# Optimization experiments

Measured on AMD Instinct MI355X. Metric: run time of the kernel, lower is better.

The kernel has to match this reference:

```python
import jax, jax.numpy as jnp
import numpy as np

NL, NH, H, FF, V, P = 12, 12, 768, 3072, 30522, 512
B, L, S = 4, 512, 8
DH = H // NH


def _layer_norm(x, g, b, eps=1e-12):
    m = x.mean(-1, keepdims=True)
    v = jnp.mean((x - m) ** 2, axis=-1, keepdims=True)
    return (x - m) * jax.lax.rsqrt(v + eps) * g + b


def setup_inputs() -> dict:
    key = jax.random.key(0)
    ks = iter(jax.random.split(key, 40))
    pm = lambda shape: jax.random.normal(next(ks), shape, jnp.float32) * 0.02
    inp = {
        'word_emb': pm((V, H)), 'pos_emb': pm((P, H)), 'type_emb': pm((2, H)),
        'emb_ln_g': jnp.ones((H,), jnp.float32), 'emb_ln_b': jnp.zeros((H,), jnp.float32),
        'Wq': pm((NL, H, H)), 'bq': jnp.zeros((NL, H), jnp.float32),
        'Wk': pm((NL, H, H)), 'bk': jnp.zeros((NL, H), jnp.float32),
        'Wv': pm((NL, H, H)), 'bv': jnp.zeros((NL, H), jnp.float32),
        'Wo': pm((NL, H, H)), 'bo': jnp.zeros((NL, H), jnp.float32),
        'attn_ln_g': jnp.ones((NL, H), jnp.float32), 'attn_ln_b': jnp.zeros((NL, H), jnp.float32),
        'W1': pm((NL, H, FF)), 'b1': jnp.zeros((NL, FF), jnp.float32),
        'W2': pm((NL, FF, H)), 'b2': jnp.zeros((NL, H), jnp.float32),
        'ffn_ln_g': jnp.ones((NL, H), jnp.float32), 'ffn_ln_b': jnp.zeros((NL, H), jnp.float32),
        'fc_w': pm((H,)), 'fc_b': jnp.zeros((), jnp.float32),
    }
    inp['input_ids'] = jax.random.randint(next(ks), (B, L), 0, V)
    inp['token_type_ids'] = jnp.zeros((B, L), jnp.int32)
    # valid-length prefix attention_mask and sorted bos_locations (history = 64)
    vl = np.array([384 + 16 * (i % 8) for i in range(B)])
    hist = 64
    am = (np.arange(L)[None, :] < vl[:, None]).astype(np.int32)
    bos = np.stack([hist + (np.arange(S) * (v - hist)) // S for v in vl]).astype(np.int64)
    inp['attention_mask'] = jnp.asarray(am)
    inp['bos_locations'] = jnp.asarray(bos)
    return inp


def _forward(word_emb, pos_emb, type_emb, emb_ln_g, emb_ln_b,
             Wq, bq, Wk, bk, Wv, bv, Wo, bo, attn_ln_g, attn_ln_b,
             W1, b1, W2, b2, ffn_ln_g, ffn_ln_b, fc_w, fc_b,
             input_ids, token_type_ids, attention_mask, bos_locations):
    Bs, Ls = input_ids.shape
    t = jnp.arange(Ls)
    valid_len = attention_mask.sum(-1)                       # [B]
    hist = bos_locations[:, 0]                               # [B] history length
    # segment id per token: number of bos positions <= t, minus 1 (-1 in history)
    seg = (bos_locations[:, :, None] <= t[None, None, :]).sum(1) - 1   # [B,L]
    valid = t[None, :] < valid_len[:, None]                  # [B,L]
    # block-diagonal candidate attention mask (history rows/cols fully visible)
    p = t[None, :, None]
    q = t[None, None, :]
    hist_pq = (p < hist[:, None, None]) | (q < hist[:, None, None])
    same_seg = seg[:, :, None] == seg[:, None, :]
    mask = valid[:, :, None] & valid[:, None, :] & (hist_pq | same_seg)  # [B,L,L]
    bias = jnp.where(mask, 0.0, -10000.0).astype(jnp.float32)[:, None, :, :]  # [B,1,L,L]

    # BERT embeddings
    x = word_emb[input_ids] + pos_emb[t][None] + type_emb[token_type_ids]
    x = _layer_norm(x, emb_ln_g, emb_ln_b)
    scale = 1.0 / jnp.sqrt(jnp.asarray(DH, x.dtype))

    for l in range(NL):
        qh = (x @ Wq[l] + bq[l]).reshape(Bs, Ls, NH, DH)
        kh = (x @ Wk[l] + bk[l]).reshape(Bs, Ls, NH, DH)
        vh = (x @ Wv[l] + bv[l]).reshape(Bs, Ls, NH, DH)
        scores = jnp.einsum('bqhd,bkhd->bhqk', qh, kh) * scale + bias
        probs = jax.nn.softmax(scores, axis=-1)
        ctx = jnp.einsum('bhqk,bkhd->bqhd', probs, vh).reshape(Bs, Ls, H)
        x = _layer_norm(x + ctx @ Wo[l] + bo[l], attn_ln_g[l], attn_ln_b[l])
        h = jax.nn.gelu(x @ W1[l] + b1[l], approximate=False)
        x = _layer_norm(x + h @ W2[l] + b2[l], ffn_ln_g[l], ffn_ln_b[l])

    # variable-length segment mean pooling via membership matmul
    starts = bos_locations                                   # [B,S]
    ends = jnp.concatenate([bos_locations[:, 1:], valid_len[:, None]], axis=1)
    memb = ((t[None, None, :] >= starts[:, :, None]) &
            (t[None, None, :] < ends[:, :, None])).astype(x.dtype)        # [B,S,L]
    pooled = jnp.einsum('bsl,bld->bsd', memb, x) / memb.sum(-1, keepdims=True)
    logits = pooled @ fc_w + fc_b                            # [B,S]
    return jnp.squeeze(logits)


def reference(word_emb, pos_emb, type_emb, emb_ln_g, emb_ln_b,
              Wq, bq, Wk, bk, Wv, bv, Wo, bo, attn_ln_g, attn_ln_b,
              W1, b1, W2, b2, ffn_ln_g, ffn_ln_b, fc_w, fc_b,
              input_ids, token_type_ids, attention_mask, bos_locations):
    return _forward(word_emb, pos_emb, type_emb, emb_ln_g, emb_ln_b,
                    Wq, bq, Wk, bk, Wv, bv, Wo, bo, attn_ln_g, attn_ln_b,
                    W1, b1, W2, b2, ffn_ln_g, ffn_ln_b, fc_w, fc_b,
                    input_ids, token_type_ids, attention_mask, bos_locations)
```

## Files before the change

### kernel.cpp

```cpp
#include <hip/hip_runtime.h>
#include <math.h>

#define HH 768
#define FF 3072
#define NL 12
#define NH 12
#define DH 64
#define BB 4
#define LL 512
#define SS 8
#define MM (BB*LL)
#define WQSZ (HH*HH)
#define W1SZ (HH*FF)
#define LWB 7077888
#define OFF_WO 1769472
#define OFF_W1 2359296
#define OFF_W2 4718592

typedef short bf16x8 __attribute__((ext_vector_type(8)));
typedef float f32x4 __attribute__((ext_vector_type(4)));

__device__ inline ushort f2b(float f) {
  unsigned u = __float_as_uint(f);
  unsigned r = (u + 0x7FFFu + ((u >> 16) & 1u)) >> 16;
  return (ushort)r;
}

__device__ inline void swz_xy(int& x, int& y) {
  int gx = gridDim.x, gy = gridDim.y;
  int flat = blockIdx.x + blockIdx.y * gx;
  int nwg = gx * gy;
  int q = nwg >> 3, r = nwg & 7;
  int xcd = flat & 7, off = flat >> 3;
  int wgid = (xcd < r ? xcd * (q + 1) : r * (q + 1) + (xcd - r) * q) + off;
  x = wgid / gy; y = wgid - x * gy;
}

__global__ void prep_kernel(const int* __restrict__ am, const int* __restrict__ bos,
                            int* __restrict__ seg, int* __restrict__ vl) {
  int b = blockIdx.x;
  int t = threadIdx.x;
  __shared__ int red[512];
  red[t] = am[b*LL + t];
  __syncthreads();
  for (int off = 256; off > 0; off >>= 1) {
    if (t < off) red[t] += red[t+off];
    __syncthreads();
  }
  if (t == 0) vl[b] = red[0];
  int cnt = 0;
  #pragma unroll
  for (int s = 0; s < SS; s++) cnt += (bos[b*SS + s] <= t) ? 1 : 0;
  seg[b*LL + t] = cnt - 1;
}

__global__ __launch_bounds__(256) void embed_ln_kernel(
    const float* __restrict__ word_emb, const float* __restrict__ pos_emb,
    const float* __restrict__ type_emb, const float* __restrict__ g,
    const float* __restrict__ bta, const int* __restrict__ ids,
    const int* __restrict__ tts, float* __restrict__ x, ushort* __restrict__ xb)
{
  int row = blockIdx.x;
  int l = row & (LL-1);
  int t = threadIdx.x;
  int id = ids[row];
  int ty = tts[row];
  float4 v = {0.f,0.f,0.f,0.f};
  float s = 0.f, sq = 0.f;
  int c = t << 2;
  if (t < 192) {
    float4 a = *(const float4*)&word_emb[(size_t)id*HH + c];
    float4 p = *(const float4*)&pos_emb[l*HH + c];
    float4 ttv = *(const float4*)&type_emb[ty*HH + c];
    v.x = a.x+p.x+ttv.x; v.y = a.y+p.y+ttv.y; v.z = a.z+p.z+ttv.z; v.w = a.w+p.w+ttv.w;
    s = v.x+v.y+v.z+v.w;
    sq = v.x*v.x+v.y*v.y+v.z*v.z+v.w*v.w;
  }
  __shared__ float rs[256], rq[256];
  rs[t] = s; rq[t] = sq;
  __syncthreads();
  for (int off = 128; off > 0; off >>= 1) {
    if (t < off) { rs[t] += rs[t+off]; rq[t] += rq[t+off]; }
    __syncthreads();
  }
  float mean = rs[0] / HH;
  float var  = rq[0] / HH - mean*mean;
  float inv  = rsqrtf(var + 1e-12f);
  if (t < 192) {
    float4 gv = *(const float4*)&g[c];
    float4 bv = *(const float4*)&bta[c];
    float4 o;
    o.x = (v.x-mean)*inv*gv.x + bv.x;
    o.y = (v.y-mean)*inv*gv.y + bv.y;
    o.z = (v.z-mean)*inv*gv.z + bv.z;
    o.w = (v.w-mean)*inv*gv.w + bv.w;
    *(float4*)&x[(size_t)row*HH + c] = o;
    ushort4 ob = { f2b(o.x), f2b(o.y), f2b(o.z), f2b(o.w) };
    *(ushort4*)&xb[(size_t)row*HH + c] = ob;
  }
}

template<int NP>
__global__ __launch_bounds__(256) void add_ln_kernel(
    const float* __restrict__ xin, const float* __restrict__ y,
    const float* __restrict__ g, const float* __restrict__ bta,
    float* __restrict__ xout, ushort* __restrict__ xb)
{
  int row = blockIdx.x;
  int t = threadIdx.x;
  float4 v = {0.f,0.f,0.f,0.f};
  float s = 0.f, sq = 0.f;
  int c = t << 2;
  size_t ix = (size_t)row*HH + c;
  if (t < 192) {
    v = *(const float4*)&xin[ix];
    #pragma unroll
    for (int p = 0; p < NP; p++) {
      float4 yv = *(const float4*)&y[(size_t)p*MM*HH + ix];
      v.x += yv.x; v.y += yv.y; v.z += yv.z; v.w += yv.w;
    }
    s = v.x+v.y+v.z+v.w;
    sq = v.x*v.x+v.y*v.y+v.z*v.z+v.w*v.w;
  }
  __shared__ float rs[256], rq[256];
  rs[t] = s; rq[t] = sq;
  __syncthreads();
  for (int off = 128; off > 0; off >>= 1) {
    if (t < off) { rs[t] += rs[t+off]; rq[t] += rq[t+off]; }
    __syncthreads();
  }
  float mean = rs[0] / HH;
  float var  = rq[0] / HH - mean*mean;
  float inv  = rsqrtf(var + 1e-12f);
  if (t < 192) {
    float4 gv = *(const float4*)&g[c];
    float4 bv = *(const float4*)&bta[c];
    float4 o;
    o.x = (v.x-mean)*inv*gv.x + bv.x;
    o.y = (v.y-mean)*inv*gv.y + bv.y;
    o.z = (v.z-mean)*inv*gv.z + bv.z;
    o.w = (v.w-mean)*inv*gv.w + bv.w;
    *(float4*)&xout[ix] = o;
    ushort4 ob = { f2b(o.x), f2b(o.y), f2b(o.z), f2b(o.w) };
    *(ushort4*)&xb[ix] = ob;
  }
}

__global__ __launch_bounds__(256) void convw_all_kernel(
    const float* __restrict__ Wq, const float* __restrict__ Wk,
    const float* __restrict__ Wv, const float* __restrict__ Wo,
    const float* __restrict__ W1, const float* __restrict__ W2,
    ushort* __restrict__ wbuf)
{
  int idx = blockIdx.x;
  int l = idx / 432;
  int t0 = idx % 432;
  size_t base = (size_t)l * LWB;
  const float* src; ushort* dst; int Nsrc, dstK, k0b, n0src, n0dst;
  if (t0 < 108) {
    int nt = t0 / 3, ktg = t0 % 3;
    int z = nt / 12, ntl = nt % 12;
    src = (z == 0 ? Wq : z == 1 ? Wk : Wv) + (size_t)l*WQSZ;
    dst = wbuf + base;
    Nsrc = HH; dstK = HH; k0b = ktg*256; n0src = ntl*64; n0dst = nt*64;
  } else if (t0 < 144) {
    int t = t0 - 108; int nt = t / 3, ktg = t % 3;
    src = Wo + (size_t)l*WQSZ;
    dst = wbuf + base + OFF_WO;
    Nsrc = HH; dstK = HH; k0b = ktg*256; n0src = n0dst = nt*64;
  } else if (t0 < 288) {
    int t = t0 - 144; int nt = t / 3, ktg = t % 3;
    src = W1 + (size_t)l*W1SZ;
    dst = wbuf + base + OFF_W1;
    Nsrc = FF; dstK = HH; k0b = ktg*256; n0src = n0dst = nt*64;
  } else {
    int t = t0 - 288; int nt = t / 12, ktg = t % 12;
    src = W2 + (size_t)l*W1SZ;
    dst = wbuf + base + OFF_W2;
    Nsrc = HH; dstK = FF; k0b = ktg*256; n0src = n0dst = nt*64;
  }
  __shared__ ushort tt[4][64][66];
  int tid = threadIdx.x;
  int kr = tid >> 4;
  int nn0 = (tid & 15) << 2;
  #pragma unroll
  for (int ti = 0; ti < 4; ti++) {
    int k0 = k0b + ti*64;
    #pragma unroll
    for (int i = 0; i < 4; i++) {
      int k = kr + i*16;
      float4 v = *(const float4*)&src[(size_t)(k0+k)*Nsrc + n0src + nn0];
      ushort2 lo = { f2b(v.x), f2b(v.y) };
      ushort2 hi = { f2b(v.z), f2b(v.w) };
      *(ushort2*)&tt[ti][k][nn0]     = lo;
      *(ushort2*)&tt[ti][k][nn0 + 2] = hi;
    }
  }
  __syncthreads();
  #pragma unroll
  for (int it = 0; it < 2; it++) {
    int n  = it*32 + (tid >> 3);
    int kc = (tid & 7) << 3;
    #pragma unroll
    for (int ti = 0; ti < 4; ti++) {
      ushort tmp8[8];
      #pragma unroll
      for (int j = 0; j < 8; j++) tmp8[j] = tt[ti][kc + j][n];
      *(uint4*)&dst[(size_t)(n0dst + n)*dstK + k0b + ti*64 + kc] = *(const uint4*)tmp8;
    }
  }
}

template<int MODE>
__global__ __launch_bounds__(256) void gemm_bt(
    const ushort* __restrict__ A, const ushort* __restrict__ Bt,
    const float* __restrict__ ba, const float* __restrict__ bb,
    const float* __restrict__ bc, float* __restrict__ Cf,
    ushort* __restrict__ Cb, int M, int N, int K)
{
  __shared__ __align__(16) ushort As[2][128*64];
  __shared__ __align__(16) ushort Bs[2][64*64];
  const int tid = threadIdx.x;
  const int lane = tid & 63, wid = tid >> 6;
  const int wm = wid >> 1, wn = wid & 1;
  int bx, by; swz_xy(bx, by);
  const int m0 = by * 128, n0 = bx * 64;
  int kbeg = 0, kcnt = K;
  if (MODE == 2) { kcnt = K >> 2; kbeg = blockIdx.z * kcnt; }
  const int NT = kcnt >> 6;

  auto STAGE = [&](int buf, int k0) {
    #pragma unroll
    for (int j = 0; j < 4; j++) {
      int c = j*256 + tid;
      int r = c >> 3;
      int kk = ((c & 7) ^ (r & 7)) << 3;
      __builtin_amdgcn_global_load_lds(
        (const __attribute__((address_space(1))) void*)(A + (size_t)(m0+r)*K + k0 + kk),
        (__attribute__((address_space(3))) void*)(&As[buf][c*8]), 16, 0, 0);
    }
    #pragma unroll
    for (int j = 0; j < 2; j++) {
      int c = j*256 + tid;
      int r = c >> 3;
      int kk = ((c & 7) ^ (r & 7)) << 3;
      __builtin_amdgcn_global_load_lds(
        (const __attribute__((address_space(1))) void*)(Bt + (size_t)(n0+r)*K + k0 + kk),
        (__attribute__((address_space(3))) void*)(&Bs[buf][c*8]), 16, 0, 0);
    }
  };

  f32x4 acc[4][2] = {};
  STAGE(0, kbeg);
  __syncthreads();
  int cur = 0;
  for (int t = 0; t < NT; ++t) {
    if (t + 1 < NT) STAGE(cur ^ 1, kbeg + (t+1)*64);
    bf16x8 af[4][2], bfv[2][2];
    #pragma unroll
    for (int mi = 0; mi < 4; mi++) {
      int row = wm*64 + mi*16 + (lane & 15);
      #pragma unroll
      for (int ks = 0; ks < 2; ks++) {
        int kb = (ks*64 + ((lane >> 4) << 4)) ^ ((row & 7) << 4);
        af[mi][ks] = *(const bf16x8*)((const char*)&As[cur][0] + row*128 + kb);
      }
    }
    #pragma unroll
    for (int ni = 0; ni < 2; ni++) {
      int row = wn*32 + ni*16 + (lane & 15);
      #pragma unroll
      for (int ks = 0; ks < 2; ks++) {
        int kb = (ks*64 + ((lane >> 4) << 4)) ^ ((row & 7) << 4);
        bfv[ni][ks] = *(const bf16x8*)((const char*)&Bs[cur][0] + row*128 + kb);
      }
    }
    #pragma unroll
    for (int ks = 0; ks < 2; ks++)
      #pragma unroll
      for (int mi = 0; mi < 4; mi++)
        #pragma unroll
        for (int ni = 0; ni < 2; ni++)
          acc[mi][ni] = __builtin_amdgcn_mfma_f32_16x16x32_bf16(af[mi][ks], bfv[ni][ks], acc[mi][ni], 0, 0, 0);
    __syncthreads();
    cur ^= 1;
  }

  #pragma unroll
  for (int mi = 0; mi < 4; mi++) {
    #pragma unroll
    for (int ni = 0; ni < 2; ni++) {
      int col = n0 + wn*32 + ni*16 + (lane & 15);
      if (MODE == 0) {
        int z = n0 / 768;
        int cc = col - z*768;
        float bvv = (z == 0 ? ba : z == 1 ? bb : bc)[cc];
        #pragma unroll
        for (int r = 0; r < 4; r++) {
          int row = m0 + wm*64 + mi*16 + (lane >> 4)*4 + r;
          Cb[(size_t)z*MM*HH + (size_t)row*HH + cc] = f2b(acc[mi][ni][r] + bvv);
        }
      } else if (MODE == 1) {
        float bvv = ba[col];
        #pragma unroll
        for (int r = 0; r < 4; r++) {
          int row = m0 + wm*64 + mi*16 + (lane >> 4)*4 + r;
          float v = acc[mi][ni][r] + bvv;
          v = 0.5f * v * (1.0f + erff(v * 0.70710678118654752f));
          Cb[(size_t)row*N + col] = f2b(v);
        }
      } else {
        float bvv = (blockIdx.z == 0) ? ba[col] : 0.f;
        #pragma unroll
        for (int r = 0; r < 4; r++) {
          int row = m0 + wm*64 + mi*16 + (lane >> 4)*4 + r;
          Cf[(size_t)blockIdx.z*M*N + (size_t)row*N + col] = acc[mi][ni][r] + bvv;
        }
      }
    }
  }
}

__global__ __launch_bounds__(256) void attn_mfma_kernel(
    const ushort* __restrict__ Q, const ushort* __restrict__ Kp, const ushort* __restrict__ Vp,
    ushort* __restrict__ ctx, const int* __restrict__ seg, const int* __restrict__ vl,
    const int* __restrict__ bos)
{
  const int q0 = blockIdx.x * 64;
  const int h  = blockIdx.y;
  const int b  = blockIdx.z;
  const int tid = threadIdx.x;
  const int lane = tid & 63;
  const int wid = tid >> 6;

  __shared__ __align__(16) char Ks[2][8192];
  __shared__ __align__(16) char Vt[2][8192];
  __shared__ __align__(16) char Ps[4][2048];
  __shared__ int segk[2][64];

  const int qrow_frag = q0 + wid*16 + (lane & 15);
  bf16x8 qf[2];
  #pragma unroll
  for (int c = 0; c < 2; c++)
    qf[c] = *(const bf16x8*)&Q[((size_t)(b*LL + qrow_frag))*HH + h*DH + 32*c + (lane >> 4)*8];

  const int vlb  = vl[b];
  const int hist = bos[b*SS];
  int segq[4]; bool qvalid[4], qhist[4];
  #pragma unroll
  for (int r = 0; r < 4; r++) {
    int qg = q0 + wid*16 + (lane >> 4)*4 + r;
    segq[r]   = seg[b*LL + qg];
    qvalid[r] = qg < vlb;
    qhist[r]  = qg < hist;
  }

  float mrow[4], lrow[4];
  #pragma unroll
  for (int r = 0; r < 4; r++) { mrow[r] = -1e30f; lrow[r] = 0.f; }
  f32x4 Oacc[4] = {};

  uint4 kreg0, kreg1, vreg0, vreg1;
  int sreg = 0;

  auto LOADT = [&](int k0) {
    int rk = tid >> 3;
    int c8 = (tid & 7) * 8;
    kreg0 = *(const uint4*)&Kp[((size_t)(b*LL + k0 + rk))*HH + h*DH + c8];
    kreg1 = *(const uint4*)&Kp[((size_t)(b*LL + k0 + rk + 32))*HH + h*DH + c8];
    vreg0 = *(const uint4*)&Vp[((size_t)(b*LL + k0 + lane))*HH + h*DH + wid*8];
    vreg1 = *(const uint4*)&Vp[((size_t)(b*LL + k0 + lane))*HH + h*DH + wid*8 + 32];
    if (tid < 64) sreg = seg[b*LL + k0 + tid];
  };
  auto STORET = [&](int buf) {
    int rk = tid >> 3;
    int c8 = (tid & 7) * 8;
    *(uint4*)(Ks[buf] + (rk*128 + ((c8*2) ^ ((rk & 7) << 4)))) = kreg0;
    int rk2 = rk + 32;
    *(uint4*)(Ks[buf] + (rk2*128 + ((c8*2) ^ ((rk2 & 7) << 4)))) = kreg1;
    const ushort* pv0 = (const ushort*)&vreg0;
    const ushort* pv1 = (const ushort*)&vreg1;
    #pragma unroll
    for (int j = 0; j < 8; j++) {
      int d  = wid*8 + j;
      *(ushort*)(Vt[buf] + (d*128 + ((lane*2) ^ ((d & 7) << 4)))) = pv0[j];
      int d2 = d + 32;
      *(ushort*)(Vt[buf] + (d2*128 + ((lane*2) ^ ((d2 & 7) << 4)))) = pv1[j];
    }
    if (tid < 64) segk[buf][tid] = sreg;
  };

  LOADT(0);
  STORET(0);
  __syncthreads();

  for (int kt = 0; kt < 8; kt++) {
    const int cur = kt & 1;
    const int k0 = kt * 64;
    if (kt < 7) LOADT(k0 + 64);
    __builtin_amdgcn_sched_barrier(0);

    f32x4 sacc[4] = {};
    #pragma unroll
    for (int t = 0; t < 4; t++) {
      int krow = (lane & 15) + 16*t;
      #pragma unroll
      for (int c = 0; c < 2; c++) {
        bf16x8 kf = *(const bf16x8*)(Ks[cur] + (krow*128 +
                      (((32*c + (lane >> 4)*8)*2) ^ ((krow & 7) << 4))));
        sacc[t] = __builtin_amdgcn_mfma_f32_16x16x32_bf16(qf[c], kf, sacc[t], 0, 0, 0);
      }
    }

    #pragma unroll
    for (int t = 0; t < 4; t++) {
      int kg = k0 + (lane & 15) + 16*t;
      bool kvalid = kg < vlb;
      bool khist  = kg < hist;
      int  sk     = segk[cur][(lane & 15) + 16*t];
      #pragma unroll
      for (int r = 0; r < 4; r++) {
        bool ok = qvalid[r] && kvalid && (khist || qhist[r] || (segq[r] == sk));
        sacc[t][r] = sacc[t][r]*0.125f + (ok ? 0.f : -10000.f);
      }
    }

    float scl[4];
    #pragma unroll
    for (int r = 0; r < 4; r++) {
      float rm = fmaxf(fmaxf(sacc[0][r], sacc[1][r]), fmaxf(sacc[2][r], sacc[3][r]));
      rm = fmaxf(rm, __shfl_xor(rm, 1));
      rm = fmaxf(rm, __shfl_xor(rm, 2));
      rm = fmaxf(rm, __shfl_xor(rm, 4));
      rm = fmaxf(rm, __shfl_xor(rm, 8));
      float mnew = (rm > mrow[r] + 8.f) ? rm : mrow[r];
      scl[r] = (mnew == mrow[r]) ? 1.f : __expf(mrow[r] - mnew);
      float rsum = 0.f;
      #pragma unroll
      for (int t = 0; t < 4; t++) {
        float p = __expf(sacc[t][r] - mnew);
        sacc[t][r] = p;
        rsum += p;
      }
      rsum += __shfl_xor(rsum, 1);
      rsum += __shfl_xor(rsum, 2);
      rsum += __shfl_xor(rsum, 4);
      rsum += __shfl_xor(rsum, 8);
      mrow[r] = mnew;
      lrow[r] = lrow[r]*scl[r] + rsum;
    }

    char* Pl = Ps[wid];
    #pragma unroll
    for (int t = 0; t < 4; t++) {
      #pragma unroll
      for (int r = 0; r < 4; r++) {
        int q = (lane >> 4)*4 + r;
        int k = (lane & 15) + 16*t;
        *(ushort*)(Pl + (q*128 + ((k*2) ^ ((q & 7) << 4)))) = f2b(sacc[t][r]);
      }
    }
    asm volatile("s_waitcnt lgkmcnt(0)" ::: "memory");
    bf16x8 pf[2];
    #pragma unroll
    for (int c = 0; c < 2; c++) {
      int q = lane & 15;
      int k = 32*c + (lane >> 4)*8;
      pf[c] = *(const bf16x8*)(Pl + (q*128 + ((k*2) ^ ((q & 7) << 4))));
    }

    bool needscale = (scl[0] != 1.f) | (scl[1] != 1.f) | (scl[2] != 1.f) | (scl[3] != 1.f);
    #pragma unroll
    for (int nt = 0; nt < 4; nt++) {
      if (needscale) {
        #pragma unroll
        for (int r = 0; r < 4; r++) Oacc[nt][r] *= scl[r];
      }
      int d = (lane & 15) + 16*nt;
      #pragma unroll
      for (int c = 0; c < 2; c++) {
        int k = 32*c + (lane >> 4)*8;
        bf16x8 vf = *(const bf16x8*)(Vt[cur] + (d*128 + ((k*2) ^ ((d & 7) << 4))));
        Oacc[nt] = __builtin_amdgcn_mfma_f32_16x16x32_bf16(pf[c], vf, Oacc[nt], 0, 0, 0);
      }
    }

    if (kt < 7) STORET(cur ^ 1);
    __syncthreads();
  }

  #pragma unroll
  for (int nt = 0; nt < 4; nt++) {
    #pragma unroll
    for (int r = 0; r < 4; r++) {
      int q = q0 + wid*16 + (lane >> 4)*4 + r;
      int d = h*DH + (lane & 15) + 16*nt;
      ctx[(size_t)(b*LL + q)*HH + d] = f2b(Oacc[nt][r] / lrow[r]);
    }
  }
}

__global__ __launch_bounds__(256) void rowdot_kernel(const float* __restrict__ x,
                                                     const float* __restrict__ w,
                                                     float* __restrict__ rd) {
  int row = blockIdx.x;
  int t = threadIdx.x;
  float s = 0.f;
  if (t < 192) {
    int c = t << 2;
    float4 xv = *(const float4*)&x[(size_t)row*HH + c];
    float4 wv = *(const float4*)&w[c];
    s = xv.x*wv.x + xv.y*wv.y + xv.z*wv.z + xv.w*wv.w;
  }
  __shared__ float red[256];
  red[t] = s;
  __syncthreads();
  for (int off = 128; off > 0; off >>= 1) {
    if (t < off) red[t] += red[t+off];
    __syncthreads();
  }
  if (t == 0) rd[row] = red[0];
}

__global__ void logits_kernel(const float* __restrict__ rd, const int* __restrict__ bos,
                              const int* __restrict__ vl, const float* __restrict__ fcb,
                              float* __restrict__ out) {
  int i = threadIdx.x;
  if (i >= BB*SS) return;
  int b = i / SS, s = i % SS;
  int start = bos[b*SS + s];
  int end   = (s == SS-1) ? vl[b] : bos[b*SS + s + 1];
  float sum = 0.f;
  for (int t = start; t < end; t++) sum += rd[b*LL + t];
  out[i] = sum / (float)(end - start) + fcb[0];
}

extern "C" void kernel_launch(void* const* d_in, const int* in_sizes, int n_in,
                              void* d_out, int out_size, void* d_ws, size_t ws_size,
                              hipStream_t stream) {
  const float* word_emb  = (const float*)d_in[0];
  const float* pos_emb   = (const float*)d_in[1];
  const float* type_emb  = (const float*)d_in[2];
  const float* emb_ln_g  = (const float*)d_in[3];
  const float* emb_ln_b  = (const float*)d_in[4];
  const float* Wq        = (const float*)d_in[5];
  const float* bq        = (const float*)d_in[6];
  const float* Wk        = (const float*)d_in[7];
  const float* bk        = (const float*)d_in[8];
  const float* Wv        = (const float*)d_in[9];
  const float* bv        = (const float*)d_in[10];
  const float* Wo        = (const float*)d_in[11];
  const float* bo        = (const float*)d_in[12];
  const float* attn_ln_g = (const float*)d_in[13];
  const float* attn_ln_b = (const float*)d_in[14];
  const float* W1        = (const float*)d_in[15];
  const float* b1        = (const float*)d_in[16];
  const float* W2        = (const float*)d_in[17];
  const float* b2        = (const float*)d_in[18];
  const float* ffn_ln_g  = (const float*)d_in[19];
  const float* ffn_ln_b  = (const float*)d_in[20];
  const float* fc_w      = (const float*)d_in[21];
  const float* fc_b      = (const float*)d_in[22];
  const int* input_ids   = (const int*)d_in[23];
  const int* token_type  = (const int*)d_in[24];
  const int* am          = (const int*)d_in[25];
  const int* bos         = (const int*)d_in[26];
  float* out = (float*)d_out;

  char* w = (char*)d_ws;
  float*  x       = (float*)w;  w += (size_t)MM*HH*4;
  float*  tmp     = (float*)w;  w += (size_t)4*MM*HH*4;
  ushort* qkv_bf  = (ushort*)w; w += (size_t)3*MM*HH*2;
  ushort* x_bf    = (ushort*)w; w += (size_t)MM*HH*2;
  ushort* ctx_bf  = (ushort*)w; w += (size_t)MM*HH*2;
  ushort* hbuf_bf = (ushort*)w; w += (size_t)MM*FF*2;
  ushort* wbuf    = (ushort*)w; w += (size_t)NL*LWB*2;
  float*  rd      = (float*)w;  w += (size_t)MM*4;
  int*    seg     = (int*)w;    w += (size_t)MM*4;
  int*    vl      = (int*)w;    w += 64;

  prep_kernel<<<BB, 512, 0, stream>>>(am, bos, seg, vl);
  convw_all_kernel<<<NL*432, 256, 0, stream>>>(Wq, Wk, Wv, Wo, W1, W2, wbuf);
  embed_ln_kernel<<<MM, 256, 0, stream>>>(word_emb, pos_emb, type_emb,
                                          emb_ln_g, emb_ln_b, input_ids, token_type, x, x_bf);

  dim3 gqkv(2304/64, MM/128);
  dim3 g_ff1(FF/64, MM/128);
  dim3 g_sk(HH/64, MM/128, 4);
  dim3 gattn(LL/64, NH, BB);

  for (int l = 0; l < NL; l++) {
    const ushort* Wqkv_t = wbuf + (size_t)l*LWB;
    const ushort* Wo_t   = wbuf + (size_t)l*LWB + OFF_WO;
    const ushort* W1_t   = wbuf + (size_t)l*LWB + OFF_W1;
    const ushort* W2_t   = wbuf + (size_t)l*LWB + OFF_W2;

    gemm_bt<0><<<gqkv, 256, 0, stream>>>(x_bf, Wqkv_t,
        bq + (size_t)l*HH, bk + (size_t)l*HH, bv + (size_t)l*HH,
        nullptr, qkv_bf, MM, 2304, HH);

    attn_mfma_kernel<<<gattn, 256, 0, stream>>>(qkv_bf, qkv_bf + (size_t)MM*HH,
                                                qkv_bf + (size_t)2*MM*HH, ctx_bf, seg, vl, bos);

    gemm_bt<2><<<g_sk, 256, 0, stream>>>(ctx_bf, Wo_t,
        bo + (size_t)l*HH, nullptr, nullptr, tmp, nullptr, MM, HH, HH);

    add_ln_kernel<4><<<MM, 256, 0, stream>>>(x, tmp, attn_ln_g + (size_t)l*HH,
                                             attn_ln_b + (size_t)l*HH, x, x_bf);

    gemm_bt<1><<<g_ff1, 256, 0, stream>>>(x_bf, W1_t,
        b1 + (size_t)l*FF, nullptr, nullptr, nullptr, hbuf_bf, MM, FF, HH);

    gemm_bt<2><<<g_sk, 256, 0, stream>>>(hbuf_bf, W2_t,
        b2 + (size_t)l*HH, nullptr, nullptr, tmp, nullptr, MM, HH, FF);

    add_ln_kernel<4><<<MM, 256, 0, stream>>>(x, tmp, ffn_ln_g + (size_t)l*HH,
                                             ffn_ln_b + (size_t)l*HH, x, x_bf);
  }

  rowdot_kernel<<<MM, 256, 0, stream>>>(x, fc_w, rd);
  logits_kernel<<<1, 64, 0, stream>>>(rd, bos, vl, fc_b, out);
}
```

Baseline: 1.429 ms.

## Tile weight layout, cut split-K to two, store partial sums as bf16

Weights are now stored as contiguous 64x64 tiles, so each B-tile load in the GEMM reads one contiguous 8KB block instead of strided rows. The split-K factor for the Wo and W2 GEMMs drops from 4 to 2, and the partial sums are written as bf16 instead of fp32. This cuts the partial-sum traffic through add_ln by about four times. In exchange, the split-K GEMMs launch half as many blocks, and rounding the partials to bf16 loses some accuracy in the residual sum.

Result: no change. 1.439 ms (+0.7%).

```diff
diff --git a/kernel.cpp b/kernel.cpp
--- a/kernel.cpp
+++ b/kernel.cpp
@@ -24,6 +24,9 @@
   unsigned u = __float_as_uint(f);
   unsigned r = (u + 0x7FFFu + ((u >> 16) & 1u)) >> 16;
   return (ushort)r;
+}
+__device__ inline float b2f(ushort b) {
+  return __uint_as_float(((unsigned)b) << 16);
 }
 
 __device__ inline void swz_xy(int& x, int& y) {
@@ -102,7 +105,7 @@
 
 template<int NP>
 __global__ __launch_bounds__(256) void add_ln_kernel(
-    const float* __restrict__ xin, const float* __restrict__ y,
+    const float* __restrict__ xin, const ushort* __restrict__ y,
     const float* __restrict__ g, const float* __restrict__ bta,
     float* __restrict__ xout, ushort* __restrict__ xb)
 {
@@ -116,8 +119,8 @@
     v = *(const float4*)&xin[ix];
     #pragma unroll
     for (int p = 0; p < NP; p++) {
-      float4 yv = *(const float4*)&y[(size_t)p*MM*HH + ix];
-      v.x += yv.x; v.y += yv.y; v.z += yv.z; v.w += yv.w;
+      ushort4 yb = *(const ushort4*)&y[(size_t)p*MM*HH + ix];
+      v.x += b2f(yb.x); v.y += b2f(yb.y); v.z += b2f(yb.z); v.w += b2f(yb.w);
     }
     s = v.x+v.y+v.z+v.w;
     sq = v.x*v.x+v.y*v.y+v.z*v.z+v.w*v.w;
@@ -153,61 +156,55 @@
     ushort* __restrict__ wbuf)
 {
   int idx = blockIdx.x;
-  int l = idx / 432;
-  int t0 = idx % 432;
+  int l = idx / 1728;
+  int t0 = idx % 1728;
   size_t base = (size_t)l * LWB;
-  const float* src; ushort* dst; int Nsrc, dstK, k0b, n0src, n0dst;
-  if (t0 < 108) {
-    int nt = t0 / 3, ktg = t0 % 3;
+  const float* src; ushort* dst; int Nsrc, dstK, k0, n0src, n0dst;
+  if (t0 < 432) {
+    int nt = t0 / 12, kt = t0 % 12;
     int z = nt / 12, ntl = nt % 12;
     src = (z == 0 ? Wq : z == 1 ? Wk : Wv) + (size_t)l*WQSZ;
     dst = wbuf + base;
-    Nsrc = HH; dstK = HH; k0b = ktg*256; n0src = ntl*64; n0dst = nt*64;
-  } else if (t0 < 144) {
-    int t = t0 - 108; int nt = t / 3, ktg = t % 3;
+    Nsrc = HH; dstK = HH; k0 = kt*64; n0src = ntl*64; n0dst = nt*64;
+  } else if (t0 < 576) {
+    int t = t0 - 432; int nt = t / 12, kt = t % 12;
     src = Wo + (size_t)l*WQSZ;
     dst = wbuf + base + OFF_WO;
-    Nsrc = HH; dstK = HH; k0b = ktg*256; n0src = n0dst = nt*64;
-  } else if (t0 < 288) {
-    int t = t0 - 144; int nt = t / 3, ktg = t % 3;
+    Nsrc = HH; dstK = HH; k0 = kt*64; n0src = n0dst = nt*64;
+  } else if (t0 < 1152) {
+    int t = t0 - 576; int nt = t / 12, kt = t % 12;
     src = W1 + (size_t)l*W1SZ;
     dst = wbuf + base + OFF_W1;
-    Nsrc = FF; dstK = HH; k0b = ktg*256; n0src = n0dst = nt*64;
+    Nsrc = FF; dstK = HH; k0 = kt*64; n0src = n0dst = nt*64;
   } else {
-    int t = t0 - 288; int nt = t / 12, ktg = t % 12;
+    int t = t0 - 1152; int nt = t / 48, kt = t % 48;
     src = W2 + (size_t)l*W1SZ;
     dst = wbuf + base + OFF_W2;
-    Nsrc = HH; dstK = FF; k0b = ktg*256; n0src = n0dst = nt*64;
-  }
-  __shared__ ushort tt[4][64][66];
+    Nsrc = HH; dstK = FF; k0 = kt*64; n0src = n0dst = nt*64;
+  }
+  __shared__ ushort tt[64][66];
   int tid = threadIdx.x;
   int kr = tid >> 4;
   int nn0 = (tid & 15) << 2;
   #pragma unroll
-  for (int ti = 0; ti < 4; ti++) {
-    int k0 = k0b + ti*64;
-    #pragma unroll
-    for (int i = 0; i < 4; i++) {
-      int k = kr + i*16;
-      float4 v = *(const float4*)&src[(size_t)(k0+k)*Nsrc + n0src + nn0];
-      ushort2 lo = { f2b(v.x), f2b(v.y) };
-      ushort2 hi = { f2b(v.z), f2b(v.w) };
-      *(ushort2*)&tt[ti][k][nn0]     = lo;
-      *(ushort2*)&tt[ti][k][nn0 + 2] = hi;
-    }
+  for (int i = 0; i < 4; i++) {
+    int k = kr + i*16;
+    float4 v = *(const float4*)&src[(size_t)(k0+k)*Nsrc + n0src + nn0];
+    ushort2 lo = { f2b(v.x), f2b(v.y) };
+    ushort2 hi = { f2b(v.z), f2b(v.w) };
+    *(ushort2*)&tt[k][nn0]     = lo;
+    *(ushort2*)&tt[k][nn0 + 2] = hi;
   }
   __syncthreads();
+  ushort* dtile = dst + ((size_t)(n0dst >> 6)*(dstK >> 6) + (k0 >> 6)) * 4096;
   #pragma unroll
   for (int it = 0; it < 2; it++) {
     int n  = it*32 + (tid >> 3);
     int kc = (tid & 7) << 3;
-    #pragma unroll
-    for (int ti = 0; ti < 4; ti++) {
-      ushort tmp8[8];
-      #pragma unroll
-      for (int j = 0; j < 8; j++) tmp8[j] = tt[ti][kc + j][n];
-      *(uint4*)&dst[(size_t)(n0dst + n)*dstK + k0b + ti*64 + kc] = *(const uint4*)tmp8;
-    }
+    ushort tmp8[8];
+    #pragma unroll
+    for (int j = 0; j < 8; j++) tmp8[j] = tt[kc + j][n];
+    *(uint4*)&dtile[n*64 + kc] = *(const uint4*)tmp8;
   }
 }
 
@@ -226,8 +223,9 @@
   int bx, by; swz_xy(bx, by);
   const int m0 = by * 128, n0 = bx * 64;
   int kbeg = 0, kcnt = K;
-  if (MODE == 2) { kcnt = K >> 2; kbeg = blockIdx.z * kcnt; }
+  if (MODE == 2) { kcnt = K >> 1; kbeg = blockIdx.z * kcnt; }
   const int NT = kcnt >> 6;
+  const ushort* Bpanel = Bt + (size_t)(n0 >> 6) * (K >> 6) * 4096;
 
   auto STAGE = [&](int buf, int k0) {
     #pragma unroll
@@ -239,13 +237,14 @@
         (const __attribute__((address_space(1))) void*)(A + (size_t)(m0+r)*K + k0 + kk),
         (__attribute__((address_space(3))) void*)(&As[buf][c*8]), 16, 0, 0);
     }
+    const ushort* btile = Bpanel + (size_t)(k0 >> 6) * 4096;
     #pragma unroll
     for (int j = 0; j < 2; j++) {
       int c = j*256 + tid;
       int r = c >> 3;
       int kk = ((c & 7) ^ (r & 7)) << 3;
       __builtin_amdgcn_global_load_lds(
-        (const __attribute__((address_space(1))) void*)(Bt + (size_t)(n0+r)*K + k0 + kk),
+        (const __attribute__((address_space(1))) void*)(btile + r*64 + kk),
         (__attribute__((address_space(3))) void*)(&Bs[buf][c*8]), 16, 0, 0);
     }
   };
@@ -314,7 +313,7 @@
         #pragma unroll
         for (int r = 0; r < 4; r++) {
           int row = m0 + wm*64 + mi*16 + (lane >> 4)*4 + r;
-          Cf[(size_t)blockIdx.z*M*N + (size_t)row*N + col] = acc[mi][ni][r] + bvv;
+          Cb[(size_t)blockIdx.z*M*N + (size_t)row*N + col] = f2b(acc[mi][ni][r] + bvv);
         }
       }
     }
@@ -569,7 +568,7 @@
 
   char* w = (char*)d_ws;
   float*  x       = (float*)w;  w += (size_t)MM*HH*4;
-  float*  tmp     = (float*)w;  w += (size_t)4*MM*HH*4;
+  ushort* tmpb    = (ushort*)w; w += (size_t)2*MM*HH*2;
   ushort* qkv_bf  = (ushort*)w; w += (size_t)3*MM*HH*2;
   ushort* x_bf    = (ushort*)w; w += (size_t)MM*HH*2;
   ushort* ctx_bf  = (ushort*)w; w += (size_t)MM*HH*2;
@@ -580,13 +579,13 @@
   int*    vl      = (int*)w;    w += 64;
 
   prep_kernel<<<BB, 512, 0, stream>>>(am, bos, seg, vl);
-  convw_all_kernel<<<NL*432, 256, 0, stream>>>(Wq, Wk, Wv, Wo, W1, W2, wbuf);
+  convw_all_kernel<<<NL*1728, 256, 0, stream>>>(Wq, Wk, Wv, Wo, W1, W2, wbuf);
   embed_ln_kernel<<<MM, 256, 0, stream>>>(word_emb, pos_emb, type_emb,
                                           emb_ln_g, emb_ln_b, input_ids, token_type, x, x_bf);
 
   dim3 gqkv(2304/64, MM/128);
   dim3 g_ff1(FF/64, MM/128);
-  dim3 g_sk(HH/64, MM/128, 4);
+  dim3 g_sk(HH/64, MM/128, 2);
   dim3 gattn(LL/64, NH, BB);
 
   for (int l = 0; l < NL; l++) {
@@ -603,18 +602,18 @@
                                                 qkv_bf + (size_t)2*MM*HH, ctx_bf, seg, vl, bos);
 
     gemm_bt<2><<<g_sk, 256, 0, stream>>>(ctx_bf, Wo_t,
-        bo + (size_t)l*HH, nullptr, nullptr, tmp, nullptr, MM, HH, HH);
-
-    add_ln_kernel<4><<<MM, 256, 0, stream>>>(x, tmp, attn_ln_g + (size_t)l*HH,
+        bo + (size_t)l*HH, nullptr, nullptr, nullptr, tmpb, MM, HH, HH);
+
+    add_ln_kernel<2><<<MM, 256, 0, stream>>>(x, tmpb, attn_ln_g + (size_t)l*HH,
                                              attn_ln_b + (size_t)l*HH, x, x_bf);
 
     gemm_bt<1><<<g_ff1, 256, 0, stream>>>(x_bf, W1_t,
         b1 + (size_t)l*FF, nullptr, nullptr, nullptr, hbuf_bf, MM, FF, HH);
 
     gemm_bt<2><<<g_sk, 256, 0, stream>>>(hbuf_bf, W2_t,
-        b2 + (size_t)l*HH, nullptr, nullptr, tmp, nullptr, MM, HH, FF);
-
-    add_ln_kernel<4><<<MM, 256, 0, stream>>>(x, tmp, ffn_ln_g + (size_t)l*HH,
+        b2 + (size_t)l*HH, nullptr, nullptr, nullptr, tmpb, MM, HH, FF);
+
+    add_ln_kernel<2><<<MM, 256, 0, stream>>>(x, tmpb, ffn_ln_g + (size_t)l*HH,
                                              ffn_ln_b + (size_t)l*HH, x, x_bf);
   }
 
```
